# Optimization experiments

Hardware: AMD Instinct MI355X
Metric: run time of the kernel (lower is better)

Reference implementation:

```python
import jax, jax.numpy as jnp
import numpy as np

# Static graph layout: B equal-sized graphs of N nodes, DEG random edges per node.
B, N, DEG = 128, 1024, 16
F_IN, H, C = 2, 64, 2
RATIO = 0.8
E = B * N * DEG
K1 = int(np.ceil(RATIO * N))      # 820
K2 = int(np.ceil(RATIO * K1))     # 656
K3 = int(np.ceil(RATIO * K2))     # 525


def setup_inputs() -> dict:
    key = jax.random.key(0)
    ks = jax.random.split(key, 24)
    x = jax.random.normal(ks[0], (B * N, F_IN), jnp.float32)
    edge_attr = jax.random.uniform(ks[1], (E,), jnp.float32)
    # per-graph random endpoints, offset so edges stay inside each graph
    local = jax.random.randint(ks[2], (2, B, N * DEG), 0, N)
    edge_index = (local + (jnp.arange(B) * N)[None, :, None]).reshape(2, E)

    def lin(k, i, o):
        return jax.random.normal(k, (i, o), jnp.float32) / np.sqrt(i)

    def bias(k, o):
        return jax.random.normal(k, (o,), jnp.float32) * 0.01

    return {
        "x": x, "edge_attr": edge_attr,
        "W1": lin(ks[3], F_IN, H), "b1": bias(ks[4], H),
        "Wp1": lin(ks[5], H, 1), "bp1": bias(ks[6], 1),
        "W2": lin(ks[7], H, H), "b2": bias(ks[8], H),
        "Wp2": lin(ks[9], H, 1), "bp2": bias(ks[10], 1),
        "W3": lin(ks[11], H, H), "b3": bias(ks[12], H),
        "Wp3": lin(ks[13], H, 1), "bp3": bias(ks[14], 1),
        "Wl1": lin(ks[15], 2 * H, H), "bl1": bias(ks[16], H),
        "Wl2": lin(ks[17], H, H // 2), "bl2": bias(ks[18], H // 2),
        "Wl3": lin(ks[19], H // 2, C), "bl3": bias(ks[20], C),
        "edge_index": edge_index,
    }


def gcn(x, src, dst, w, W, b):
    """PyG GCNConv with gcn_norm (self-loops weight 1)."""
    h = x @ W                                       # [BN, out]
    deg = jnp.zeros((x.shape[0],), x.dtype).at[dst].add(w) + 1.0
    dinv = jax.lax.rsqrt(deg)
    norm = dinv[src] * w * dinv[dst]                # [E]
    out = jnp.zeros_like(h).at[dst].add(norm[:, None] * h[src])
    out = out + (dinv * dinv)[:, None] * h          # self-loop term
    return out + b


def sagpool(x, alive, src, dst, Wp, bp, k):
    """SAGPool: unweighted GCN scoring, per-graph top-k, x <- x * tanh(score).
    Removed nodes/edges are kept as masked (alive=False) slots -> static shapes."""
    we = (alive[src] & alive[dst]).astype(x.dtype)
    score = gcn(x, src, dst, we, Wp, bp)[:, 0]      # [BN]
    s = jnp.where(alive, score, -jnp.inf).reshape(B, N)
    _, idx = jax.lax.top_k(s, k)                    # [B, k]
    alive_new = jnp.zeros((B, N), bool).at[jnp.arange(B)[:, None], idx].set(True).reshape(-1)
    xn = jnp.where(alive_new[:, None], x * jnp.tanh(score)[:, None], 0.0)
    return xn, alive_new


def readout(x, alive):
    """concat(global_max_pool, global_mean_pool) over alive nodes per graph."""
    xr = x.reshape(B, N, -1)
    m = alive.reshape(B, N, 1)
    mx = jnp.max(jnp.where(m, xr, -jnp.inf), axis=1)
    mn = jnp.sum(jnp.where(m, xr, 0.0), axis=1) / jnp.sum(m, axis=1).astype(x.dtype)
    return jnp.concatenate([mx, mn], axis=1)        # [B, 2*H]


def _forward(x, edge_attr, W1, b1, Wp1, bp1, W2, b2, Wp2, bp2, W3, b3, Wp3, bp3,
             Wl1, bl1, Wl2, bl2, Wl3, bl3, edge_index):
    src, dst = edge_index[0], edge_index[1]
    h = jax.nn.relu(gcn(x, src, dst, edge_attr, W1, b1))
    h, a1 = sagpool(h, jnp.ones((B * N,), bool), src, dst, Wp1, bp1, K1)
    x1 = readout(h, a1)

    ea1 = edge_attr * (a1[src] & a1[dst]).astype(x.dtype)
    h = jax.nn.relu(gcn(h, src, dst, ea1, W2, b2))
    h, a2 = sagpool(h, a1, src, dst, Wp2, bp2, K2)
    x2 = readout(h, a2)

    # conv3 is called WITHOUT edge_weight -> surviving edges get weight 1
    ea2 = (a2[src] & a2[dst]).astype(x.dtype)
    h = jax.nn.relu(gcn(h, src, dst, ea2, W3, b3))
    h, a3 = sagpool(h, a2, src, dst, Wp3, bp3, K3)
    x3 = readout(h, a3)

    g = x1 + x2 + x3
    g = jax.nn.relu(g @ Wl1 + bl1)                  # dropout: eval mode (identity)
    g = jax.nn.relu(g @ Wl2 + bl2)
    return jax.nn.log_softmax(g @ Wl3 + bl3, axis=-1)


def reference(x, edge_attr, W1, b1, Wp1, bp1, W2, b2, Wp2, bp2, W3, b3, Wp3, bp3,
              Wl1, bl1, Wl2, bl2, Wl3, bl3, edge_index):
    return _forward(x, edge_attr, W1, b1, Wp1, bp1, W2, b2, Wp2, bp2, W3, b3,
                    Wp3, bp3, Wl1, bl1, Wl2, bl2, Wl3, bl3, edge_index)
```

## Files before the change

### kernel.cpp

```cpp
#include <hip/hip_runtime.h>
#include <math.h>

#define NB 128
#define NN 1024
#define BNODES (NB*NN)
#define NE 2097152
#define EPG (NE/NB)
#define EPT (EPG/NN)
#define FH 64
#define KK1 820
#define KK2 656
#define KK3 525

__global__ __launch_bounds__(1024) void k_csr(const int* __restrict__ ei,
                                              const float* __restrict__ ea,
                                              int* __restrict__ rowptr,
                                              int2* __restrict__ csr_sw,
                                              float* __restrict__ dinvW,
                                              float* __restrict__ dinvU) {
  extern __shared__ int2 lcsr[];
  __shared__ int cnt[NN];
  __shared__ int cur[NN];
  __shared__ float wsum[NN];
  int b = blockIdx.x, t = threadIdx.x;
  int node = b*NN + t;
  cnt[t] = 0;
  wsum[t] = 0.f;
  __syncthreads();
  int ebase = b*EPG;
  int se[EPT]; int de[EPT]; float we[EPT];
  #pragma unroll
  for (int i = 0; i < EPT; ++i) {
    int e = ebase + i*NN + t;
    se[i] = ei[e];
    de[i] = ei[NE + e] - b*NN;
    we[i] = ea[e];
    atomicAdd(&cnt[de[i]], 1);
    atomicAdd(&wsum[de[i]], we[i]);
  }
  __syncthreads();
  int v = cnt[t];
  for (int off = 1; off < NN; off <<= 1) {
    int u = (t >= off) ? cnt[t - off] : 0;
    __syncthreads();
    cnt[t] += u;
    __syncthreads();
  }
  int excl = cnt[t] - v;
  rowptr[node] = ebase + excl;
  cur[t] = excl;
  dinvW[node] = rsqrtf(1.f + wsum[t]);
  dinvU[node] = rsqrtf(1.f + (float)v);
  if (b == NB-1 && t == NN-1) rowptr[BNODES] = NE;
  __syncthreads();
  #pragma unroll
  for (int i = 0; i < EPT; ++i) {
    int pos = atomicAdd(&cur[de[i]], 1);
    lcsr[pos] = make_int2(se[i], __float_as_int(we[i]));
  }
  __syncthreads();
  float4* dst4 = (float4*)(csr_sw + ebase);
  const float4* src4 = (const float4*)lcsr;
  #pragma unroll
  for (int i = 0; i < EPG/2/NN; ++i)
    dst4[i*NN + t] = src4[i*NN + t];
}

template<int MODE, bool L1S>
__global__ __launch_bounds__(1024, 4) void k_gath(
    const int* __restrict__ rowptr, const int2* __restrict__ csr_sw,
    const float* __restrict__ dinvW, const float* __restrict__ src,
    const float* __restrict__ Wl,
    const float* __restrict__ bias, const float* __restrict__ Wp,
    float* __restrict__ hA, float* __restrict__ qpart) {
  extern __shared__ float sHB[];
  __shared__ float sDW[NN];
  __shared__ float sWp[32];
  __shared__ float sB[32];
  __shared__ float sW1[64];
  int b = blockIdx.x >> 1, half = blockIdx.x & 1;
  int t = threadIdx.x, l8 = t & 7;
  int gbase = b*NN;
  sDW[t] = dinvW[gbase + t];
  if (t < 32) { sWp[t] = Wp[half*32 + t]; sB[t] = bias[half*32 + t]; }
  float4* sHB4 = (float4*)sHB;
  if (L1S) {
    if (t < 32) { sW1[t] = Wl[half*32 + t]; sW1[32 + t] = Wl[64 + half*32 + t]; }
    __syncthreads();
    #pragma unroll
    for (int i = 0; i < 32; ++i) {
      int el = i*1024 + t;
      int n = el >> 5, ff = el & 31;
      float x0 = src[(size_t)(gbase + n)*2];
      float x1 = src[(size_t)(gbase + n)*2 + 1];
      sHB[n*32 + ff] = x0*sW1[ff] + x1*sW1[32 + ff];
    }
  } else {
    const float4* hB4 = (const float4*)src;
    #pragma unroll
    for (int i = 0; i < 8; ++i) {
      int idx = i*1024 + t;
      int n = idx >> 3, j = idx & 7;
      sHB4[n*8 + j] = hB4[(size_t)(gbase + n)*16 + half*8 + j];
    }
  }
  __syncthreads();
  float4 bv = ((const float4*)sB)[l8];
  float4 wp = ((const float4*)sWp)[l8];
  #pragma unroll 1
  for (int pass = 0; pass < 8; ++pass) {
    int n = pass*128 + (t >> 3);
    int gn = gbase + n;
    float dd = sDW[n];
    float4 hv = sHB4[n*8 + l8];
    float dd2 = dd*dd;
    float4 acc;
    acc.x = fmaf(dd2, hv.x, bv.x);
    acc.y = fmaf(dd2, hv.y, bv.y);
    acc.z = fmaf(dd2, hv.z, bv.z);
    acc.w = fmaf(dd2, hv.w, bv.w);
    int r0 = rowptr[gn], r1 = rowptr[gn+1];
    for (int base = r0; base < r1; base += 8) {
      int sj = 0; float cj = 0.f;
      if (base + l8 < r1) {
        int2 p = csr_sw[base + l8];
        sj = p.x - gbase;
        float w = (MODE == 2) ? 1.f : __int_as_float(p.y);
        cj = sDW[sj] * w * dd;
      }
      float4 v[8];
      #pragma unroll
      for (int j = 0; j < 8; ++j) {
        int s = __shfl(sj, j, 8);
        v[j] = sHB4[s*8 + l8];
      }
      #pragma unroll
      for (int j = 0; j < 8; ++j) {
        float c = __shfl(cj, j, 8);
        acc.x = fmaf(c, v[j].x, acc.x);
        acc.y = fmaf(c, v[j].y, acc.y);
        acc.z = fmaf(c, v[j].z, acc.z);
        acc.w = fmaf(c, v[j].w, acc.w);
      }
    }
    acc.x = fmaxf(acc.x, 0.f); acc.y = fmaxf(acc.y, 0.f);
    acc.z = fmaxf(acc.z, 0.f); acc.w = fmaxf(acc.w, 0.f);
    ((float4*)hA)[(size_t)gn*16 + half*8 + l8] = acc;
    float dot = acc.x*wp.x + acc.y*wp.y + acc.z*wp.z + acc.w*wp.w;
    dot += __shfl_xor(dot, 4, 8);
    dot += __shfl_xor(dot, 2, 8);
    dot += __shfl_xor(dot, 1, 8);
    if (l8 == 0) qpart[half*BNODES + gn] = dot;
  }
}

__global__ void k_qfin(const float* __restrict__ dinvU, const float* __restrict__ qp,
                       float* __restrict__ q) {
  int i = blockIdx.x*256 + threadIdx.x;
  if (i < BNODES) q[i] = dinvU[i]*(qp[i] + qp[BNODES + i]);
}

__global__ void k_score(const int* __restrict__ rowptr, const int2* __restrict__ csr_sw,
                        const float* __restrict__ dinvU, const float* __restrict__ q,
                        const float* __restrict__ bp, float* __restrict__ score) {
  int t = threadIdx.x;
  int l16 = t & 15;
  int d = blockIdx.x*16 + (t >> 4);
  float du = dinvU[d];
  float sum = 0.f;
  if (du != 0.f) {
    int r0 = rowptr[d], r1 = rowptr[d+1];
    for (int base = r0; base < r1; base += 16)
      if (base + l16 < r1) sum += q[csr_sw[base + l16].x];
  }
  #pragma unroll
  for (int off = 8; off; off >>= 1) sum += __shfl_xor(sum, off, 16);
  if (l16 == 0) score[d] = bp[0] + du*(q[d] + sum);
}

__global__ void k_topk(const float* __restrict__ score,
                       const float* __restrict__ dinvU, int k,
                       float* __restrict__ tm, int* __restrict__ aliveN) {
  __shared__ float sc[NN];
  int b = blockIdx.x >> 2, p = blockIdx.x & 3;
  int t = threadIdx.x;
  int gbase = b*NN;
  #pragma unroll
  for (int i = 0; i < 4; ++i) {
    int n = i*256 + t;
    sc[n] = (dinvU[gbase + n] != 0.f) ? score[gbase + n] : -INFINITY;
  }
  __syncthreads();
  int n = p*256 + t;
  int node = gbase + n;
  float me = sc[n];
  float raw = score[node];
  int rank = 0;
  const float4* sc4 = (const float4*)sc;
  for (int j4 = 0; j4 < NN/4; ++j4) {
    float4 o = sc4[j4];
    int jb = j4*4;
    rank += (o.x > me) || (o.x == me && jb+0 < n);
    rank += (o.y > me) || (o.y == me && jb+1 < n);
    rank += (o.z > me) || (o.z == me && jb+2 < n);
    rank += (o.w > me) || (o.w == me && jb+3 < n);
  }
  int sel = (rank < k) ? 1 : 0;
  aliveN[node] = sel;
  tm[node] = sel ? tanhf(raw) : 0.f;
}

template<int MODE>
__global__ void k_degs(const int* __restrict__ rowptr, const int2* __restrict__ csr_sw,
                       const int* __restrict__ alive,
                       float* __restrict__ dinvW, float* __restrict__ dinvU) {
  int t = threadIdx.x;
  int l16 = t & 15;
  int d = blockIdx.x*16 + (t >> 4);
  int r0 = rowptr[d], r1 = rowptr[d+1];
  float sW = 0.f, sU = 0.f;
  for (int base = r0; base < r1; base += 16) {
    if (base + l16 < r1) {
      int2 p = csr_sw[base + l16];
      if (alive[p.x]) { sW += (MODE == 2) ? 1.f : __int_as_float(p.y); sU += 1.f; }
    }
  }
  #pragma unroll
  for (int off = 8; off; off >>= 1) {
    sW += __shfl_xor(sW, off, 16);
    sU += __shfl_xor(sU, off, 16);
  }
  if (l16 == 0) {
    bool dA = (alive[d] != 0);
    dinvW[d] = dA ? rsqrtf(1.f + sW) : 0.f;
    dinvU[d] = dA ? rsqrtf(1.f + sU) : 0.f;
  }
}

template<bool DOLIN>
__global__ void k_srl(const float* __restrict__ hA, const float* __restrict__ tm,
                      const int* __restrict__ aliveN, const float* __restrict__ W,
                      float* __restrict__ hB,
                      float* __restrict__ pmax, float* __restrict__ psum) {
  __shared__ float sX[64][65];
  __shared__ float sW[64*64];
  __shared__ int sAl[64];
  __shared__ float rm[4][FH], rs[4][FH];
  int t = threadIdx.x;
  int blk = blockIdx.x;
  int nb = blk*64;
  if (DOLIN)
    for (int i = t; i < 1024; i += 256) ((float4*)sW)[i] = ((const float4*)W)[i];
  if (t < 64) sAl[t] = aliveN[nb + t];
  #pragma unroll
  for (int i = 0; i < 16; ++i) {
    int gidx = (nb << 6) + i*256 + t;
    int node = gidx >> 6, f = gidx & 63;
    sX[node - nb][f] = hA[gidx] * tm[node];
  }
  __syncthreads();
  {
    int f = t & 63, r = t >> 6;
    float mx = -INFINITY, sm = 0.f;
    #pragma unroll
    for (int i = 0; i < 16; ++i) {
      int n = r + i*4;
      float v = sX[n][f];
      if (sAl[n]) { mx = fmaxf(mx, v); sm += v; }
    }
    rm[r][f] = mx; rs[r][f] = sm;
  }
  __syncthreads();
  if (t < FH) {
    float m2 = fmaxf(fmaxf(rm[0][t], rm[1][t]), fmaxf(rm[2][t], rm[3][t]));
    float s2 = rs[0][t] + rs[1][t] + rs[2][t] + rs[3][t];
    pmax[blk*FH + t] = m2;
    psum[blk*FH + t] = s2;
  }
  if (DOLIN) {
    int node = t >> 2;
    int f0 = (t & 3) * 16;
    float4 a0 = {0,0,0,0}, a1 = a0, a2 = a0, a3 = a0;
    #pragma unroll 4
    for (int k = 0; k < 64; ++k) {
      float xv = sX[node][k];
      const float4 w0 = *(const float4*)&sW[k*64 + f0];
      const float4 w1 = *(const float4*)&sW[k*64 + f0 + 4];
      const float4 w2 = *(const float4*)&sW[k*64 + f0 + 8];
      const float4 w3 = *(const float4*)&sW[k*64 + f0 + 12];
      a0.x = fmaf(xv, w0.x, a0.x); a0.y = fmaf(xv, w0.y, a0.y);
      a0.z = fmaf(xv, w0.z, a0.z); a0.w = fmaf(xv, w0.w, a0.w);
      a1.x = fmaf(xv, w1.x, a1.x); a1.y = fmaf(xv, w1.y, a1.y);
      a1.z = fmaf(xv, w1.z, a1.z); a1.w = fmaf(xv, w1.w, a1.w);
      a2.x = fmaf(xv, w2.x, a2.x); a2.y = fmaf(xv, w2.y, a2.y);
      a2.z = fmaf(xv, w2.z, a2.z); a2.w = fmaf(xv, w2.w, a2.w);
      a3.x = fmaf(xv, w3.x, a3.x); a3.y = fmaf(xv, w3.y, a3.y);
      a3.z = fmaf(xv, w3.z, a3.z); a3.w = fmaf(xv, w3.w, a3.w);
    }
    float4* dst = (float4*)(hB + (size_t)(nb + node)*FH + f0);
    dst[0] = a0; dst[1] = a1; dst[2] = a2; dst[3] = a3;
  }
}

__global__ void k_mlp(const float* __restrict__ pmax, const float* __restrict__ psum,
                      const float* __restrict__ Wl1, const float* __restrict__ bl1,
                      const float* __restrict__ Wl2, const float* __restrict__ bl2,
                      const float* __restrict__ Wl3, const float* __restrict__ bl3,
                      float* __restrict__ out) {
  __shared__ float sg[2*FH];
  __shared__ float l1[FH];
  __shared__ float l2[FH/2];
  __shared__ float l3[2];
  int b = blockIdx.x, t = threadIdx.x;
  const float kf[3] = {(float)KK1, (float)KK2, (float)KK3};
  float gm = 0.f, gs = 0.f;
  #pragma unroll
  for (int l = 0; l < 3; ++l) {
    const float* pm = pmax + (size_t)l*NB*16*FH + (b*16)*FH;
    const float* ps = psum + (size_t)l*NB*16*FH + (b*16)*FH;
    float mm = -INFINITY, ss = 0.f;
    #pragma unroll
    for (int p = 0; p < 16; ++p) {
      mm = fmaxf(mm, pm[p*FH + t]);
      ss += ps[p*FH + t];
    }
    gm += mm;
    gs += ss / kf[l];
  }
  sg[t] = gm;
  sg[FH + t] = gs;
  __syncthreads();
  float acc = bl1[t];
  #pragma unroll
  for (int k = 0; k < 2*FH; ++k) acc = fmaf(sg[k], Wl1[k*FH + t], acc);
  l1[t] = fmaxf(acc, 0.f);
  __syncthreads();
  if (t < 32) {
    float a2 = bl2[t];
    #pragma unroll
    for (int k = 0; k < FH; ++k) a2 = fmaf(l1[k], Wl2[k*32 + t], a2);
    l2[t] = fmaxf(a2, 0.f);
  }
  __syncthreads();
  if (t < 2) {
    float a3 = bl3[t];
    #pragma unroll
    for (int k = 0; k < 32; ++k) a3 = fmaf(l2[k], Wl3[k*2 + t], a3);
    l3[t] = a3;
  }
  __syncthreads();
  if (t == 0) {
    float m = fmaxf(l3[0], l3[1]);
    float lse = m + logf(expf(l3[0]-m) + expf(l3[1]-m));
    out[b*2+0] = l3[0] - lse;
    out[b*2+1] = l3[1] - lse;
  }
}

extern "C" void kernel_launch(void* const* d_in, const int* in_sizes, int n_in,
                              void* d_out, int out_size, void* d_ws, size_t ws_size,
                              hipStream_t stream) {
  const float* x   = (const float*)d_in[0];
  const float* ea  = (const float*)d_in[1];
  const float* W1  = (const float*)d_in[2];
  const float* b1  = (const float*)d_in[3];
  const float* Wp1 = (const float*)d_in[4];
  const float* bp1 = (const float*)d_in[5];
  const float* W2  = (const float*)d_in[6];
  const float* b2  = (const float*)d_in[7];
  const float* Wp2 = (const float*)d_in[8];
  const float* bp2 = (const float*)d_in[9];
  const float* W3  = (const float*)d_in[10];
  const float* b3  = (const float*)d_in[11];
  const float* Wp3 = (const float*)d_in[12];
  const float* bp3 = (const float*)d_in[13];
  const float* Wl1 = (const float*)d_in[14];
  const float* bl1 = (const float*)d_in[15];
  const float* Wl2 = (const float*)d_in[16];
  const float* bl2 = (const float*)d_in[17];
  const float* Wl3 = (const float*)d_in[18];
  const float* bl3 = (const float*)d_in[19];
  const int*   ei  = (const int*)d_in[20];
  float* out = (float*)d_out;

  int2* csr_sw = (int2*)d_ws;
  float* hA    = (float*)(csr_sw + NE);
  float* hB    = hA + (size_t)BNODES*FH;
  float* dinvW = hB + (size_t)BNODES*FH;
  float* dinvU = dinvW + BNODES;
  float* qpart = dinvU + BNODES;
  float* q     = qpart + 2*BNODES;
  float* score = q + BNODES;
  float* tm    = score + BNODES;
  float* pmax  = tm + BNODES;
  float* psum  = pmax + 3*NB*16*FH;
  int* aliveN  = (int*)(psum + 3*NB*16*FH);
  int* rowptr  = aliveN + BNODES;

  const size_t gathLds = (size_t)NN*32*sizeof(float);
  const int gS = BNODES/64;
  const int gG = BNODES/16;
  const int gN = BNODES/256;

  k_csr<<<NB, 1024, EPG*sizeof(int2), stream>>>(ei, ea, rowptr, csr_sw, dinvW, dinvU);

  k_gath<0,true><<<NB*2, 1024, gathLds, stream>>>(rowptr, csr_sw, dinvW, x, W1, b1, Wp1, hA, qpart);
  k_qfin<<<gN, 256, 0, stream>>>(dinvU, qpart, q);
  k_score<<<gG, 256, 0, stream>>>(rowptr, csr_sw, dinvU, q, bp1, score);
  k_topk<<<NB*4, 256, 0, stream>>>(score, dinvU, KK1, tm, aliveN);
  k_srl<true><<<gS, 256, 0, stream>>>(hA, tm, aliveN, W2, hB, pmax, psum);
  k_degs<1><<<gG, 256, 0, stream>>>(rowptr, csr_sw, aliveN, dinvW, dinvU);

  k_gath<1,false><<<NB*2, 1024, gathLds, stream>>>(rowptr, csr_sw, dinvW, hB, W1, b2, Wp2, hA, qpart);
  k_qfin<<<gN, 256, 0, stream>>>(dinvU, qpart, q);
  k_score<<<gG, 256, 0, stream>>>(rowptr, csr_sw, dinvU, q, bp2, score);
  k_topk<<<NB*4, 256, 0, stream>>>(score, dinvU, KK2, tm, aliveN);
  k_srl<true><<<gS, 256, 0, stream>>>(hA, tm, aliveN, W3, hB, pmax + NB*16*FH, psum + NB*16*FH);
  k_degs<2><<<gG, 256, 0, stream>>>(rowptr, csr_sw, aliveN, dinvW, dinvU);

  k_gath<2,false><<<NB*2, 1024, gathLds, stream>>>(rowptr, csr_sw, dinvW, hB, W1, b3, Wp3, hA, qpart);
  k_qfin<<<gN, 256, 0, stream>>>(dinvU, qpart, q);
  k_score<<<gG, 256, 0, stream>>>(rowptr, csr_sw, dinvU, q, bp3, score);
  k_topk<<<NB*4, 256, 0, stream>>>(score, dinvU, KK3, tm, aliveN);
  k_srl<false><<<gS, 256, 0, stream>>>(hA, tm, aliveN, W3, hB, pmax + 2*NB*16*FH, psum + 2*NB*16*FH);

  k_mlp<<<NB, FH, 0, stream>>>(pmax, psum, Wl1, bl1, Wl2, bl2, Wl3, bl3, out);
}
```

Measured before the change: 375.1 us.

## Split gather into feature quarters with quarter-major hidden-state layout

The GCN gather kernel now splits each graph's 64 features into four 16-wide quarters instead of two halves. This halves shared memory per block and doubles the grid, which raises the launch-bounds occupancy target. Hidden states hA and hB are stored quarter-major, so each block loads its slice contiguously. k_srl and k_qfin are adapted to the new layout and four partial score sums. The trade-off is that each block re-reads the CSR edge lists and rowptr, so edge traffic doubles in exchange for occupancy and contiguous loads.

```diff
diff --git a/kernel.cpp b/kernel.cpp
--- a/kernel.cpp
+++ b/kernel.cpp
@@ -67,7 +67,7 @@
 }
 
 template<int MODE, bool L1S>
-__global__ __launch_bounds__(1024, 4) void k_gath(
+__global__ __launch_bounds__(1024, 8) void k_gath(
     const int* __restrict__ rowptr, const int2* __restrict__ csr_sw,
     const float* __restrict__ dinvW, const float* __restrict__ src,
     const float* __restrict__ Wl,
@@ -75,44 +75,43 @@
     float* __restrict__ hA, float* __restrict__ qpart) {
   extern __shared__ float sHB[];
   __shared__ float sDW[NN];
-  __shared__ float sWp[32];
-  __shared__ float sB[32];
-  __shared__ float sW1[64];
-  int b = blockIdx.x >> 1, half = blockIdx.x & 1;
-  int t = threadIdx.x, l8 = t & 7;
+  __shared__ float sWp[16];
+  __shared__ float sB[16];
+  __shared__ float sW1[32];
+  int b = blockIdx.x >> 2, quarter = blockIdx.x & 3;
+  int t = threadIdx.x, l4 = t & 3;
   int gbase = b*NN;
   sDW[t] = dinvW[gbase + t];
-  if (t < 32) { sWp[t] = Wp[half*32 + t]; sB[t] = bias[half*32 + t]; }
+  if (t < 16) { sWp[t] = Wp[quarter*16 + t]; sB[t] = bias[quarter*16 + t]; }
   float4* sHB4 = (float4*)sHB;
   if (L1S) {
-    if (t < 32) { sW1[t] = Wl[half*32 + t]; sW1[32 + t] = Wl[64 + half*32 + t]; }
+    if (t < 16) { sW1[t] = Wl[quarter*16 + t]; sW1[16 + t] = Wl[64 + quarter*16 + t]; }
     __syncthreads();
     #pragma unroll
-    for (int i = 0; i < 32; ++i) {
+    for (int i = 0; i < 16; ++i) {
       int el = i*1024 + t;
-      int n = el >> 5, ff = el & 31;
+      int n = el >> 4, ff = el & 15;
       float x0 = src[(size_t)(gbase + n)*2];
       float x1 = src[(size_t)(gbase + n)*2 + 1];
-      sHB[n*32 + ff] = x0*sW1[ff] + x1*sW1[32 + ff];
+      sHB[n*16 + ff] = x0*sW1[ff] + x1*sW1[16 + ff];
     }
   } else {
-    const float4* hB4 = (const float4*)src;
-    #pragma unroll
-    for (int i = 0; i < 8; ++i) {
+    const float4* hq4 = (const float4*)src + (size_t)quarter*BNODES*4 + (size_t)gbase*4;
+    #pragma unroll
+    for (int i = 0; i < 4; ++i) {
       int idx = i*1024 + t;
-      int n = idx >> 3, j = idx & 7;
-      sHB4[n*8 + j] = hB4[(size_t)(gbase + n)*16 + half*8 + j];
-    }
-  }
-  __syncthreads();
-  float4 bv = ((const float4*)sB)[l8];
-  float4 wp = ((const float4*)sWp)[l8];
+      sHB4[idx] = hq4[idx];
+    }
+  }
+  __syncthreads();
+  float4 bv = ((const float4*)sB)[l4];
+  float4 wp = ((const float4*)sWp)[l4];
   #pragma unroll 1
-  for (int pass = 0; pass < 8; ++pass) {
-    int n = pass*128 + (t >> 3);
+  for (int pass = 0; pass < 4; ++pass) {
+    int n = pass*256 + (t >> 2);
     int gn = gbase + n;
     float dd = sDW[n];
-    float4 hv = sHB4[n*8 + l8];
+    float4 hv = sHB4[n*4 + l4];
     float dd2 = dd*dd;
     float4 acc;
     acc.x = fmaf(dd2, hv.x, bv.x);
@@ -120,44 +119,40 @@
     acc.z = fmaf(dd2, hv.z, bv.z);
     acc.w = fmaf(dd2, hv.w, bv.w);
     int r0 = rowptr[gn], r1 = rowptr[gn+1];
-    for (int base = r0; base < r1; base += 8) {
+    for (int base = r0; base < r1; base += 4) {
       int sj = 0; float cj = 0.f;
-      if (base + l8 < r1) {
-        int2 p = csr_sw[base + l8];
+      if (base + l4 < r1) {
+        int2 p = csr_sw[base + l4];
         sj = p.x - gbase;
         float w = (MODE == 2) ? 1.f : __int_as_float(p.y);
         cj = sDW[sj] * w * dd;
       }
-      float4 v[8];
       #pragma unroll
-      for (int j = 0; j < 8; ++j) {
-        int s = __shfl(sj, j, 8);
-        v[j] = sHB4[s*8 + l8];
-      }
-      #pragma unroll
-      for (int j = 0; j < 8; ++j) {
-        float c = __shfl(cj, j, 8);
-        acc.x = fmaf(c, v[j].x, acc.x);
-        acc.y = fmaf(c, v[j].y, acc.y);
-        acc.z = fmaf(c, v[j].z, acc.z);
-        acc.w = fmaf(c, v[j].w, acc.w);
+      for (int j = 0; j < 4; ++j) {
+        int s   = __shfl(sj, j, 4);
+        float c = __shfl(cj, j, 4);
+        float4 v = sHB4[s*4 + l4];
+        acc.x = fmaf(c, v.x, acc.x);
+        acc.y = fmaf(c, v.y, acc.y);
+        acc.z = fmaf(c, v.z, acc.z);
+        acc.w = fmaf(c, v.w, acc.w);
       }
     }
     acc.x = fmaxf(acc.x, 0.f); acc.y = fmaxf(acc.y, 0.f);
     acc.z = fmaxf(acc.z, 0.f); acc.w = fmaxf(acc.w, 0.f);
-    ((float4*)hA)[(size_t)gn*16 + half*8 + l8] = acc;
+    ((float4*)hA)[(size_t)quarter*BNODES*4 + (size_t)gn*4 + l4] = acc;
     float dot = acc.x*wp.x + acc.y*wp.y + acc.z*wp.z + acc.w*wp.w;
-    dot += __shfl_xor(dot, 4, 8);
-    dot += __shfl_xor(dot, 2, 8);
-    dot += __shfl_xor(dot, 1, 8);
-    if (l8 == 0) qpart[half*BNODES + gn] = dot;
+    dot += __shfl_xor(dot, 2, 4);
+    dot += __shfl_xor(dot, 1, 4);
+    if (l4 == 0) qpart[quarter*BNODES + gn] = dot;
   }
 }
 
 __global__ void k_qfin(const float* __restrict__ dinvU, const float* __restrict__ qp,
                        float* __restrict__ q) {
   int i = blockIdx.x*256 + threadIdx.x;
-  if (i < BNODES) q[i] = dinvU[i]*(qp[i] + qp[BNODES + i]);
+  if (i < BNODES)
+    q[i] = dinvU[i]*(qp[i] + qp[BNODES + i] + qp[2*BNODES + i] + qp[3*BNODES + i]);
 }
 
 __global__ void k_score(const int* __restrict__ rowptr, const int2* __restrict__ csr_sw,
@@ -244,6 +239,7 @@
                       float* __restrict__ pmax, float* __restrict__ psum) {
   __shared__ float sX[64][65];
   __shared__ float sW[64*64];
+  __shared__ float sTm[64];
   __shared__ int sAl[64];
   __shared__ float rm[4][FH], rs[4][FH];
   int t = threadIdx.x;
@@ -251,12 +247,17 @@
   int nb = blk*64;
   if (DOLIN)
     for (int i = t; i < 1024; i += 256) ((float4*)sW)[i] = ((const float4*)W)[i];
-  if (t < 64) sAl[t] = aliveN[nb + t];
-  #pragma unroll
-  for (int i = 0; i < 16; ++i) {
-    int gidx = (nb << 6) + i*256 + t;
-    int node = gidx >> 6, f = gidx & 63;
-    sX[node - nb][f] = hA[gidx] * tm[node];
+  if (t < 64) { sTm[t] = tm[nb + t]; sAl[t] = aliveN[nb + t]; }
+  __syncthreads();
+  #pragma unroll
+  for (int q = 0; q < 4; ++q) {
+    const float* hq = hA + (size_t)q*BNODES*16 + (size_t)nb*16;
+    #pragma unroll
+    for (int i = 0; i < 4; ++i) {
+      int idx = i*256 + t;
+      int n = idx >> 4, ff = idx & 15;
+      sX[n][q*16 + ff] = hq[idx] * sTm[n];
+    }
   }
   __syncthreads();
   {
@@ -279,7 +280,8 @@
   }
   if (DOLIN) {
     int node = t >> 2;
-    int f0 = (t & 3) * 16;
+    int quarter = t & 3;
+    int f0 = quarter * 16;
     float4 a0 = {0,0,0,0}, a1 = a0, a2 = a0, a3 = a0;
     #pragma unroll 4
     for (int k = 0; k < 64; ++k) {
@@ -297,7 +299,7 @@
       a3.x = fmaf(xv, w3.x, a3.x); a3.y = fmaf(xv, w3.y, a3.y);
       a3.z = fmaf(xv, w3.z, a3.z); a3.w = fmaf(xv, w3.w, a3.w);
     }
-    float4* dst = (float4*)(hB + (size_t)(nb + node)*FH + f0);
+    float4* dst = (float4*)(hB + (size_t)quarter*BNODES*16 + (size_t)(nb + node)*16);
     dst[0] = a0; dst[1] = a1; dst[2] = a2; dst[3] = a3;
   }
 }
@@ -389,7 +391,7 @@
   float* dinvW = hB + (size_t)BNODES*FH;
   float* dinvU = dinvW + BNODES;
   float* qpart = dinvU + BNODES;
-  float* q     = qpart + 2*BNODES;
+  float* q     = qpart + 4*BNODES;
   float* score = q + BNODES;
   float* tm    = score + BNODES;
   float* pmax  = tm + BNODES;
@@ -397,28 +399,28 @@
   int* aliveN  = (int*)(psum + 3*NB*16*FH);
   int* rowptr  = aliveN + BNODES;
 
-  const size_t gathLds = (size_t)NN*32*sizeof(float);
+  const size_t gathLds = (size_t)NN*16*sizeof(float);
   const int gS = BNODES/64;
   const int gG = BNODES/16;
   const int gN = BNODES/256;
 
   k_csr<<<NB, 1024, EPG*sizeof(int2), stream>>>(ei, ea, rowptr, csr_sw, dinvW, dinvU);
 
-  k_gath<0,true><<<NB*2, 1024, gathLds, stream>>>(rowptr, csr_sw, dinvW, x, W1, b1, Wp1, hA, qpart);
+  k_gath<0,true><<<NB*4, 1024, gathLds, stream>>>(rowptr, csr_sw, dinvW, x, W1, b1, Wp1, hA, qpart);
   k_qfin<<<gN, 256, 0, stream>>>(dinvU, qpart, q);
   k_score<<<gG, 256, 0, stream>>>(rowptr, csr_sw, dinvU, q, bp1, score);
   k_topk<<<NB*4, 256, 0, stream>>>(score, dinvU, KK1, tm, aliveN);
   k_srl<true><<<gS, 256, 0, stream>>>(hA, tm, aliveN, W2, hB, pmax, psum);
   k_degs<1><<<gG, 256, 0, stream>>>(rowptr, csr_sw, aliveN, dinvW, dinvU);
 
-  k_gath<1,false><<<NB*2, 1024, gathLds, stream>>>(rowptr, csr_sw, dinvW, hB, W1, b2, Wp2, hA, qpart);
+  k_gath<1,false><<<NB*4, 1024, gathLds, stream>>>(rowptr, csr_sw, dinvW, hB, W1, b2, Wp2, hA, qpart);
   k_qfin<<<gN, 256, 0, stream>>>(dinvU, qpart, q);
   k_score<<<gG, 256, 0, stream>>>(rowptr, csr_sw, dinvU, q, bp2, score);
   k_topk<<<NB*4, 256, 0, stream>>>(score, dinvU, KK2, tm, aliveN);
   k_srl<true><<<gS, 256, 0, stream>>>(hA, tm, aliveN, W3, hB, pmax + NB*16*FH, psum + NB*16*FH);
   k_degs<2><<<gG, 256, 0, stream>>>(rowptr, csr_sw, aliveN, dinvW, dinvU);
 
-  k_gath<2,false><<<NB*2, 1024, gathLds, stream>>>(rowptr, csr_sw, dinvW, hB, W1, b3, Wp3, hA, qpart);
+  k_gath<2,false><<<NB*4, 1024, gathLds, stream>>>(rowptr, csr_sw, dinvW, hB, W1, b3, Wp3, hA, qpart);
   k_qfin<<<gN, 256, 0, stream>>>(dinvU, qpart, q);
   k_score<<<gG, 256, 0, stream>>>(rowptr, csr_sw, dinvU, q, bp3, score);
   k_topk<<<NB*4, 256, 0, stream>>>(score, dinvU, KK3, tm, aliveN);
```

Result: no change. 376.5 us (+0.4%).
